# Performance work log

Measured on AMD Instinct MI355X. Metric: run time of the kernel, lower is better.

## Reference

```python
import jax, jax.numpy as jnp
import numpy as np

ITER_NUM = 3
BN_EPS = 1e-5
L2_EPS = 1e-12


def setup_inputs() -> dict:
    key = jax.random.key(0)
    k1, k2 = jax.random.split(key, 2)
    B, C, h, w = 64, 256, 14, 14
    E = 512
    feat = jax.random.normal(k1, (B, C, h, w), dtype=jnp.float32)
    W_proj = jax.random.normal(k2, (E, C * C), dtype=jnp.float32) * (1.0 / np.sqrt(C * C))
    b_proj = jnp.zeros((E,), dtype=jnp.float32)
    bn_gamma = jnp.ones((E,), dtype=jnp.float32)
    bn_beta = jnp.zeros((E,), dtype=jnp.float32)
    bn_mean = jnp.zeros((E,), dtype=jnp.float32)
    bn_var = jnp.ones((E,), dtype=jnp.float32)
    return {"feat": feat, "W_proj": W_proj, "b_proj": b_proj,
            "bn_gamma": bn_gamma, "bn_beta": bn_beta,
            "bn_mean": bn_mean, "bn_var": bn_var}


def _mpncov(feat):
    # feat: [B, C, h, w] -> [B, C, C] matrix square root of normalized covariance
    B, C, h, w = feat.shape
    M = h * w
    x = feat.reshape(B, C, M)
    # I_hat = I - (1/M) * ones  (centering matrix)
    I_hat = jnp.eye(M, dtype=feat.dtype) - (1.0 / M) * jnp.ones((M, M), dtype=feat.dtype)
    # y = x @ I_hat @ x^T / M  -> [B, C, C]
    xc = jnp.einsum('bcm,mn->bcn', x, I_hat)
    y = jnp.einsum('bcm,bdm->bcd', xc, x) / M
    trY = jnp.trace(y, axis1=-2, axis2=-1)  # [B]
    y = y / trY[:, None, None]
    I = jnp.broadcast_to(jnp.eye(C, dtype=feat.dtype), (B, C, C))
    Y, Z = y, I
    for _ in range(ITER_NUM):
        ZY = jnp.einsum('bij,bjk->bik', Z, Y)
        T = 3.0 * I - ZY
        Y = 0.5 * jnp.einsum('bij,bjk->bik', Y, T)
        Z = 0.5 * jnp.einsum('bij,bjk->bik', T, Z)
    return Y * jnp.sqrt(trY)[:, None, None]


def _l2_normalize(x, axis=-1):
    n = jnp.sqrt(jnp.sum(x * x, axis=axis, keepdims=True))
    return x / jnp.maximum(n, L2_EPS)


def reference(feat, W_proj, b_proj, bn_gamma, bn_beta, bn_mean, bn_var):
    B = feat.shape[0]
    pooled = _mpncov(feat)                      # [B, C, C]
    flat = pooled.reshape(B, -1)                # [B, C*C]
    flat = _l2_normalize(flat, axis=1)
    # dropout in eval mode = identity
    emb = flat @ W_proj.T + b_proj              # [B, E]
    # BatchNorm1d (inference mode, running stats)
    emb = (emb - bn_mean) * jax.lax.rsqrt(bn_var + BN_EPS) * bn_gamma + bn_beta
    norm_embedding = _l2_normalize(emb, axis=1)
    return norm_embedding
```

## Files before the change

### kernel.cpp

```cpp
#include <hip/hip_runtime.h>
#include <hip/hip_bf16.h>

#define BATCH 64
#define CDIM  256
#define MHW   196
#define MP    224
#define EDIM  512
#define CC    65536
#define NTRI  10

typedef __attribute__((ext_vector_type(8))) short short8_t;
typedef __attribute__((ext_vector_type(4))) float f32x4;
typedef __attribute__((ext_vector_type(4))) unsigned int u32x4;

static __device__ __forceinline__ short f2bf(float f) {
    __hip_bfloat16 h = __float2bfloat16(f);
    return (short)__builtin_bit_cast(unsigned short, h);
}

struct MMOp {
    const __hip_bfloat16* A;
    const __hip_bfloat16* B;
    const __hip_bfloat16* D;
    __hip_bfloat16*       out;
    const float*          alpha_ptr;
    int                   alpha_mode;
    float                 alpha_c, beta, gamma;
    float*                nrm;
};

__global__ __launch_bounds__(256) void k_center(const float* __restrict__ feat,
                                                __hip_bfloat16* __restrict__ xcb,
                                                float* __restrict__ rowsq)
{
    const int row = blockIdx.x * 4 + (threadIdx.x >> 6);
    const int l = threadIdx.x & 63;
    const float* src = feat + (size_t)row * MHW;
    float v0 = src[l];
    float v1 = src[l + 64];
    float v2 = src[l + 128];
    float v3 = (l + 192 < MHW) ? src[l + 192] : 0.0f;
    float s = v0 + v1 + v2 + v3;
    #pragma unroll
    for (int o = 32; o >= 1; o >>= 1) s += __shfl_xor(s, o, 64);
    const float mean = s * (1.0f / MHW);
    v0 -= mean; v1 -= mean; v2 -= mean;
    v3 = (l + 192 < MHW) ? (v3 - mean) : 0.0f;
    float sq = v0*v0 + v1*v1 + v2*v2 + v3*v3;
    #pragma unroll
    for (int o = 32; o >= 1; o >>= 1) sq += __shfl_xor(sq, o, 64);
    if (l == 0) rowsq[row] = sq;
    __hip_bfloat16* dst = xcb + (size_t)row * MP;
    dst[l]       = __float2bfloat16(v0);
    dst[l + 64]  = __float2bfloat16(v1);
    dst[l + 128] = __float2bfloat16(v2);
    if (l + 192 < MP) dst[l + 192] = __float2bfloat16(v3);
}

template<int KT, bool NORM>
__global__ __launch_bounds__(256) void k_mm(MMOp op0, MMOp op1)
{
    const MMOp& op = (blockIdx.y == 0) ? op0 : op1;

    __shared__ __hip_bfloat16 As[64][72];
    __shared__ __hip_bfloat16 Bs[64][72];
    __shared__ float red[4];
    __shared__ float s_alpha;

    const int b = blockIdx.x / NTRI;
    const int t = blockIdx.x - b * NTRI;
    int ti, tj;
    if (t < 4)      { ti = 0; tj = t; }
    else if (t < 7) { ti = 1; tj = t - 3; }
    else if (t < 9) { ti = 2; tj = t - 5; }
    else            { ti = 3; tj = 3; }

    const int tid = threadIdx.x;
    const int wv = tid >> 6, l = tid & 63;
    const int wr = wv >> 1, wc = wv & 1;
    const int lr = l & 15,  lg = l >> 4;

    if (op.alpha_mode) {
        float v = op.alpha_ptr[b * 256 + tid];
        #pragma unroll
        for (int o = 32; o >= 1; o >>= 1) v += __shfl_xor(v, o, 64);
        if (l == 0) red[wv] = v;
        __syncthreads();
        if (tid == 0) s_alpha = op.alpha_c / (red[0] + red[1] + red[2] + red[3]);
    } else if (tid == 0) {
        s_alpha = op.alpha_c;
    }

    const __hip_bfloat16* Ab = op.A + (size_t)b * (CDIM * KT) + (size_t)ti * 64 * KT;
    const __hip_bfloat16* Bb = op.B + (size_t)b * (CDIM * KT) + (size_t)tj * 64 * KT;

    f32x4 acc[2][2];
    #pragma unroll
    for (int i = 0; i < 2; i++)
        #pragma unroll
        for (int j = 0; j < 2; j++)
            #pragma unroll
            for (int r = 0; r < 4; r++) acc[i][j][r] = 0.0f;

    #pragma unroll
    for (int k0 = 0; k0 < KT; k0 += 64) {
        const int kw   = (KT - k0 >= 64) ? 64 : (KT - k0);
        const int segs = kw >> 3;
        __syncthreads();
        for (int u = tid; u < 64 * segs; u += 256) {
            const int row = u / segs;
            const int seg = u - row * segs;
            *reinterpret_cast<u32x4*>(&As[row][seg * 8]) =
                *reinterpret_cast<const u32x4*>(Ab + (size_t)row * KT + k0 + seg * 8);
            *reinterpret_cast<u32x4*>(&Bs[row][seg * 8]) =
                *reinterpret_cast<const u32x4*>(Bb + (size_t)row * KT + k0 + seg * 8);
        }
        __syncthreads();
        const int nks = kw >> 5;
        for (int ks = 0; ks < nks; ks++) {
            short8_t af[2], bfr[2];
            #pragma unroll
            for (int i = 0; i < 2; i++)
                af[i] = *reinterpret_cast<const short8_t*>(&As[wr * 32 + i * 16 + lr][ks * 32 + lg * 8]);
            #pragma unroll
            for (int j = 0; j < 2; j++)
                bfr[j] = *reinterpret_cast<const short8_t*>(&Bs[wc * 32 + j * 16 + lr][ks * 32 + lg * 8]);
            #pragma unroll
            for (int i = 0; i < 2; i++)
                #pragma unroll
                for (int j = 0; j < 2; j++)
                    acc[i][j] = __builtin_amdgcn_mfma_f32_16x16x32_bf16(af[i], bfr[j], acc[i][j], 0, 0, 0);
        }
    }

    const float a = s_alpha;
    __hip_bfloat16* ob = op.out + (size_t)b * CC;
    const __hip_bfloat16* Db = op.D ? (op.D + (size_t)b * CC) : nullptr;
    float ns = 0.0f;
    #pragma unroll
    for (int i = 0; i < 2; i++) {
        #pragma unroll
        for (int j = 0; j < 2; j++) {
            #pragma unroll
            for (int r = 0; r < 4; r++) {
                const int grow = ti * 64 + wr * 32 + i * 16 + lg * 4 + r;
                const int gcol = tj * 64 + wc * 32 + j * 16 + lr;
                float v = a * acc[i][j][r];
                if (Db) v += op.beta * __bfloat162float(Db[grow * 256 + gcol]);
                if (grow == gcol) v += op.gamma;
                const __hip_bfloat16 hv = __float2bfloat16(v);
                ob[grow * 256 + gcol] = hv;
                if (ti != tj) ob[gcol * 256 + grow] = hv;
                if (NORM) {
                    const float fv = __bfloat162float(hv);
                    ns += ((ti != tj) ? 2.0f : 1.0f) * fv * fv;
                }
            }
        }
    }
    if constexpr (NORM) {
        #pragma unroll
        for (int o = 32; o >= 1; o >>= 1) ns += __shfl_xor(ns, o, 64);
        __syncthreads();
        if (l == 0) red[wv] = ns;
        __syncthreads();
        if (tid == 0) op.nrm[b * NTRI + t] = red[0] + red[1] + red[2] + red[3];
    }
}

__global__ __launch_bounds__(256) void k_proj(const __hip_bfloat16* __restrict__ flat,
                                              const float* __restrict__ W,
                                              float* __restrict__ upart)
{
    const int ks = blockIdx.x;
    const int et = blockIdx.y;
    const int tid = threadIdx.x, wv = tid >> 6, l = tid & 63;
    const int lr = l & 15, lg = l >> 4;
    const int kbase = ks * 2048 + wv * 512;

    f32x4 acc[4][4];
    #pragma unroll
    for (int i = 0; i < 4; i++)
        #pragma unroll
        for (int j = 0; j < 4; j++)
            #pragma unroll
            for (int r = 0; r < 4; r++) acc[i][j][r] = 0.0f;

    for (int kk = 0; kk < 512; kk += 32) {
        const int k = kbase + kk + lg * 8;
        short8_t af[4];
        #pragma unroll
        for (int i = 0; i < 4; i++)
            af[i] = *reinterpret_cast<const short8_t*>(flat + (size_t)(i * 16 + lr) * CC + k);
        short8_t bfr[4];
        #pragma unroll
        for (int j = 0; j < 4; j++) {
            const f32x4* wp = reinterpret_cast<const f32x4*>(W + (size_t)(et * 64 + j * 16 + lr) * CC + k);
            const f32x4 w0 = wp[0], w1 = wp[1];
            short8_t s;
            s[0] = f2bf(w0[0]); s[1] = f2bf(w0[1]); s[2] = f2bf(w0[2]); s[3] = f2bf(w0[3]);
            s[4] = f2bf(w1[0]); s[5] = f2bf(w1[1]); s[6] = f2bf(w1[2]); s[7] = f2bf(w1[3]);
            bfr[j] = s;
        }
        #pragma unroll
        for (int i = 0; i < 4; i++)
            #pragma unroll
            for (int j = 0; j < 4; j++)
                acc[i][j] = __builtin_amdgcn_mfma_f32_16x16x32_bf16(af[i], bfr[j], acc[i][j], 0, 0, 0);
    }

    __shared__ float racc[2][64][65];
    if (wv >= 2) {
        #pragma unroll
        for (int i = 0; i < 4; i++)
            #pragma unroll
            for (int j = 0; j < 4; j++)
                #pragma unroll
                for (int r = 0; r < 4; r++)
                    racc[wv - 2][i * 16 + lg * 4 + r][j * 16 + lr] = acc[i][j][r];
    }
    __syncthreads();
    if (wv < 2) {
        #pragma unroll
        for (int i = 0; i < 4; i++)
            #pragma unroll
            for (int j = 0; j < 4; j++)
                #pragma unroll
                for (int r = 0; r < 4; r++)
                    racc[wv][i * 16 + lg * 4 + r][j * 16 + lr] += acc[i][j][r];
    }
    __syncthreads();
    float* ub = upart + (size_t)ks * (64 * EDIM);
    #pragma unroll
    for (int q = 0; q < 16; q++) {
        const int idx = q * 256 + tid;
        const int x = idx >> 6, y = idx & 63;
        ub[(size_t)x * EDIM + et * 64 + y] = racc[0][x][y] + racc[1][x][y];
    }
}

__global__ __launch_bounds__(512) void k_final(const float* __restrict__ upart,
                                               const float* __restrict__ nrmp,
                                               const float* __restrict__ bias,
                                               const float* __restrict__ gma,
                                               const float* __restrict__ bta,
                                               const float* __restrict__ mu,
                                               const float* __restrict__ var,
                                               float* __restrict__ out)
{
    const int b = blockIdx.x;
    const int e = threadIdx.x;
    float u = 0.0f;
    for (int p = 0; p < 32; p++)
        u += upart[((size_t)p * 64 + b) * EDIM + e];
    float fro = 0.0f;
    #pragma unroll
    for (int q = 0; q < NTRI; q++) fro += nrmp[b * NTRI + q];
    const float s = 1.0f / fmaxf(sqrtf(fro), 1e-12f);
    const float emb = s * u + bias[e];
    const float v = (emb - mu[e]) * rsqrtf(var[e] + 1e-5f) * gma[e] + bta[e];
    float sq = v * v;
    #pragma unroll
    for (int o = 32; o >= 1; o >>= 1) sq += __shfl_xor(sq, o, 64);
    __shared__ float wsum[8];
    if ((e & 63) == 0) wsum[e >> 6] = sq;
    __syncthreads();
    float tot = 0.0f;
    #pragma unroll
    for (int i = 0; i < 8; i++) tot += wsum[i];
    out[(size_t)b * EDIM + e] = v / fmaxf(sqrtf(tot), 1e-12f);
}

extern "C" void kernel_launch(void* const* d_in, const int* in_sizes, int n_in,
                              void* d_out, int out_size, void* d_ws, size_t ws_size,
                              hipStream_t stream)
{
    const float* feat = (const float*)d_in[0];
    const float* W    = (const float*)d_in[1];
    const float* bias = (const float*)d_in[2];
    const float* gma  = (const float*)d_in[3];
    const float* bta  = (const float*)d_in[4];
    const float* mu   = (const float*)d_in[5];
    const float* var  = (const float*)d_in[6];
    float* out = (float*)d_out;

    char* ws = (char*)d_ws;
    constexpr size_t XCB_BYTES = (size_t)BATCH * CDIM * MP * 2;
    constexpr size_t MATB      = (size_t)BATCH * CC * 2;
    constexpr size_t OFF_ROWSQ = 4096;
    constexpr size_t OFF_XCB   = OFF_ROWSQ + (size_t)BATCH * CDIM * 4;
    constexpr size_t OFF_M     = OFF_XCB + XCB_BYTES;
    constexpr size_t OFF_UP    = OFF_M + 5 * MATB;
    constexpr size_t NEEDED    = OFF_UP + (size_t)32 * 64 * EDIM * 4;
    if (ws_size < NEEDED) return;

    float* nrmp  = (float*)(ws + 1024);
    float* rowsq = (float*)(ws + OFF_ROWSQ);
    __hip_bfloat16* xcb = (__hip_bfloat16*)(ws + OFF_XCB);
    __hip_bfloat16* M0  = (__hip_bfloat16*)(ws + OFF_M + 0 * MATB);
    __hip_bfloat16* M1  = (__hip_bfloat16*)(ws + OFF_M + 1 * MATB);
    __hip_bfloat16* M2  = (__hip_bfloat16*)(ws + OFF_M + 2 * MATB);
    __hip_bfloat16* M3  = (__hip_bfloat16*)(ws + OFF_M + 3 * MATB);
    __hip_bfloat16* M4  = (__hip_bfloat16*)(ws + OFF_M + 4 * MATB);
    float* upart = (float*)(ws + OFF_UP);

    k_center<<<dim3(4096), dim3(256), 0, stream>>>(feat, xcb, rowsq);

    const dim3 g1(BATCH * NTRI, 1), g2(BATCH * NTRI, 2), blk(256);
    MMOp nop = {};

    MMOp cov = {xcb, xcb, nullptr, M0, rowsq, 1, 1.0f, 0.0f, 0.0f, nullptr};
    k_mm<MP, false><<<g1, blk, 0, stream>>>(cov, nop);
    MMOp y1 = {M0, M0, M0, M1, nullptr, 0, -0.5f, 1.5f, 0.0f, nullptr};
    k_mm<256, false><<<g1, blk, 0, stream>>>(y1, nop);
    MMOp t2 = {M0, M1, M1, M2, nullptr, 0, 0.5f, -1.5f, 3.0f, nullptr};
    k_mm<256, false><<<g1, blk, 0, stream>>>(t2, nop);
    MMOp y2 = {M1, M2, nullptr, M3, nullptr, 0, 0.5f, 0.0f, 0.0f, nullptr};
    MMOp z2 = {M2, M0, M2, M4, nullptr, 0, -0.25f, 0.75f, 0.0f, nullptr};
    k_mm<256, false><<<g2, blk, 0, stream>>>(y2, z2);
    MMOp t3 = {M4, M3, nullptr, M1, nullptr, 0, -1.0f, 0.0f, 3.0f, nullptr};
    k_mm<256, false><<<g1, blk, 0, stream>>>(t3, nop);
    MMOp y3 = {M3, M1, nullptr, M2, nullptr, 0, 0.5f, 0.0f, 0.0f, nrmp};
    k_mm<256, true ><<<g1, blk, 0, stream>>>(y3, nop);

    k_proj<<<dim3(32, 8), blk, 0, stream>>>(M2, W, upart);
    k_final<<<dim3(64), 512, 0, stream>>>(upart, nrmp, bias, gma, bta, mu, var, out);
}
```

Measured before the change: 133.1 us.

## Fuse centering and Newton-Schulz chain into one per-batch megakernel with W pre-conversion

New measurement: 287.5 us. +116.0%, slower.

```diff
diff --git a/kernel.cpp b/kernel.cpp
--- a/kernel.cpp
+++ b/kernel.cpp
@@ -8,34 +8,21 @@
 #define EDIM  512
 #define CC    65536
 #define NTRI  10
+#define WCONV_BLOCKS 2048
 
 typedef __attribute__((ext_vector_type(8))) short short8_t;
 typedef __attribute__((ext_vector_type(4))) float f32x4;
-typedef __attribute__((ext_vector_type(4))) unsigned int u32x4;
-
-static __device__ __forceinline__ short f2bf(float f) {
+
+static __device__ __forceinline__ unsigned short f2bfu(float f) {
     __hip_bfloat16 h = __float2bfloat16(f);
-    return (short)__builtin_bit_cast(unsigned short, h);
-}
-
-struct MMOp {
-    const __hip_bfloat16* A;
-    const __hip_bfloat16* B;
-    const __hip_bfloat16* D;
-    __hip_bfloat16*       out;
-    const float*          alpha_ptr;
-    int                   alpha_mode;
-    float                 alpha_c, beta, gamma;
-    float*                nrm;
-};
-
-__global__ __launch_bounds__(256) void k_center(const float* __restrict__ feat,
-                                                __hip_bfloat16* __restrict__ xcb,
-                                                float* __restrict__ rowsq)
-{
-    const int row = blockIdx.x * 4 + (threadIdx.x >> 6);
-    const int l = threadIdx.x & 63;
-    const float* src = feat + (size_t)row * MHW;
+    return __builtin_bit_cast(unsigned short, h);
+}
+
+static __device__ __forceinline__ void center_row(
+    const float* __restrict__ feat_b, __hip_bfloat16* __restrict__ xcb_b,
+    float* __restrict__ rs, int row, int l)
+{
+    const float* src = feat_b + (size_t)row * MHW;
     float v0 = src[l];
     float v1 = src[l + 64];
     float v2 = src[l + 128];
@@ -49,8 +36,8 @@
     float sq = v0*v0 + v1*v1 + v2*v2 + v3*v3;
     #pragma unroll
     for (int o = 32; o >= 1; o >>= 1) sq += __shfl_xor(sq, o, 64);
-    if (l == 0) rowsq[row] = sq;
-    __hip_bfloat16* dst = xcb + (size_t)row * MP;
+    if (l == 0) rs[row] = sq;
+    __hip_bfloat16* dst = xcb_b + (size_t)row * MP;
     dst[l]       = __float2bfloat16(v0);
     dst[l + 64]  = __float2bfloat16(v1);
     dst[l + 128] = __float2bfloat16(v2);
@@ -58,99 +45,59 @@
 }
 
 template<int KT, bool NORM>
-__global__ __launch_bounds__(256) void k_mm(MMOp op0, MMOp op1)
-{
-    const MMOp& op = (blockIdx.y == 0) ? op0 : op1;
-
-    __shared__ __hip_bfloat16 As[64][72];
-    __shared__ __hip_bfloat16 Bs[64][72];
-    __shared__ float red[4];
-    __shared__ float s_alpha;
-
-    const int b = blockIdx.x / NTRI;
-    const int t = blockIdx.x - b * NTRI;
+static __device__ __forceinline__ float mm64(
+    const __hip_bfloat16* __restrict__ A, const __hip_bfloat16* __restrict__ Bm,
+    const __hip_bfloat16* __restrict__ D, __hip_bfloat16* __restrict__ out,
+    float a, float beta, float gamma, int t, int l)
+{
     int ti, tj;
     if (t < 4)      { ti = 0; tj = t; }
     else if (t < 7) { ti = 1; tj = t - 3; }
     else if (t < 9) { ti = 2; tj = t - 5; }
     else            { ti = 3; tj = 3; }
-
-    const int tid = threadIdx.x;
-    const int wv = tid >> 6, l = tid & 63;
-    const int wr = wv >> 1, wc = wv & 1;
-    const int lr = l & 15,  lg = l >> 4;
-
-    if (op.alpha_mode) {
-        float v = op.alpha_ptr[b * 256 + tid];
-        #pragma unroll
-        for (int o = 32; o >= 1; o >>= 1) v += __shfl_xor(v, o, 64);
-        if (l == 0) red[wv] = v;
-        __syncthreads();
-        if (tid == 0) s_alpha = op.alpha_c / (red[0] + red[1] + red[2] + red[3]);
-    } else if (tid == 0) {
-        s_alpha = op.alpha_c;
-    }
-
-    const __hip_bfloat16* Ab = op.A + (size_t)b * (CDIM * KT) + (size_t)ti * 64 * KT;
-    const __hip_bfloat16* Bb = op.B + (size_t)b * (CDIM * KT) + (size_t)tj * 64 * KT;
-
-    f32x4 acc[2][2];
-    #pragma unroll
-    for (int i = 0; i < 2; i++)
-        #pragma unroll
-        for (int j = 0; j < 2; j++)
+    const int lr = l & 15, lg = l >> 4;
+
+    f32x4 acc[4][4];
+    #pragma unroll
+    for (int i = 0; i < 4; i++)
+        #pragma unroll
+        for (int j = 0; j < 4; j++)
             #pragma unroll
             for (int r = 0; r < 4; r++) acc[i][j][r] = 0.0f;
 
-    #pragma unroll
-    for (int k0 = 0; k0 < KT; k0 += 64) {
-        const int kw   = (KT - k0 >= 64) ? 64 : (KT - k0);
-        const int segs = kw >> 3;
-        __syncthreads();
-        for (int u = tid; u < 64 * segs; u += 256) {
-            const int row = u / segs;
-            const int seg = u - row * segs;
-            *reinterpret_cast<u32x4*>(&As[row][seg * 8]) =
-                *reinterpret_cast<const u32x4*>(Ab + (size_t)row * KT + k0 + seg * 8);
-            *reinterpret_cast<u32x4*>(&Bs[row][seg * 8]) =
-                *reinterpret_cast<const u32x4*>(Bb + (size_t)row * KT + k0 + seg * 8);
-        }
-        __syncthreads();
-        const int nks = kw >> 5;
-        for (int ks = 0; ks < nks; ks++) {
-            short8_t af[2], bfr[2];
-            #pragma unroll
-            for (int i = 0; i < 2; i++)
-                af[i] = *reinterpret_cast<const short8_t*>(&As[wr * 32 + i * 16 + lr][ks * 32 + lg * 8]);
-            #pragma unroll
-            for (int j = 0; j < 2; j++)
-                bfr[j] = *reinterpret_cast<const short8_t*>(&Bs[wc * 32 + j * 16 + lr][ks * 32 + lg * 8]);
-            #pragma unroll
-            for (int i = 0; i < 2; i++)
-                #pragma unroll
-                for (int j = 0; j < 2; j++)
-                    acc[i][j] = __builtin_amdgcn_mfma_f32_16x16x32_bf16(af[i], bfr[j], acc[i][j], 0, 0, 0);
-        }
-    }
-
-    const float a = s_alpha;
-    __hip_bfloat16* ob = op.out + (size_t)b * CC;
-    const __hip_bfloat16* Db = op.D ? (op.D + (size_t)b * CC) : nullptr;
+    const __hip_bfloat16* Ab = A  + (size_t)(ti * 64 + lr) * KT;
+    const __hip_bfloat16* Bb = Bm + (size_t)(tj * 64 + lr) * KT;
+    for (int k0 = 0; k0 < KT; k0 += 32) {
+        const int k = k0 + lg * 8;
+        short8_t af[4], bfr[4];
+        #pragma unroll
+        for (int i = 0; i < 4; i++)
+            af[i] = *reinterpret_cast<const short8_t*>(Ab + (size_t)i * 16 * KT + k);
+        #pragma unroll
+        for (int j = 0; j < 4; j++)
+            bfr[j] = *reinterpret_cast<const short8_t*>(Bb + (size_t)j * 16 * KT + k);
+        #pragma unroll
+        for (int i = 0; i < 4; i++)
+            #pragma unroll
+            for (int j = 0; j < 4; j++)
+                acc[i][j] = __builtin_amdgcn_mfma_f32_16x16x32_bf16(af[i], bfr[j], acc[i][j], 0, 0, 0);
+    }
+
     float ns = 0.0f;
     #pragma unroll
-    for (int i = 0; i < 2; i++) {
-        #pragma unroll
-        for (int j = 0; j < 2; j++) {
+    for (int i = 0; i < 4; i++) {
+        #pragma unroll
+        for (int j = 0; j < 4; j++) {
             #pragma unroll
             for (int r = 0; r < 4; r++) {
-                const int grow = ti * 64 + wr * 32 + i * 16 + lg * 4 + r;
-                const int gcol = tj * 64 + wc * 32 + j * 16 + lr;
+                const int grow = ti * 64 + i * 16 + lg * 4 + r;
+                const int gcol = tj * 64 + j * 16 + lr;
                 float v = a * acc[i][j][r];
-                if (Db) v += op.beta * __bfloat162float(Db[grow * 256 + gcol]);
-                if (grow == gcol) v += op.gamma;
+                if (D) v += beta * __bfloat162float(D[grow * 256 + gcol]);
+                if (grow == gcol) v += gamma;
                 const __hip_bfloat16 hv = __float2bfloat16(v);
-                ob[grow * 256 + gcol] = hv;
-                if (ti != tj) ob[gcol * 256 + grow] = hv;
+                out[grow * 256 + gcol] = hv;
+                if (ti != tj) out[gcol * 256 + grow] = hv;
                 if (NORM) {
                     const float fv = __bfloat162float(hv);
                     ns += ((ti != tj) ? 2.0f : 1.0f) * fv * fv;
@@ -158,25 +105,95 @@
             }
         }
     }
-    if constexpr (NORM) {
-        #pragma unroll
-        for (int o = 32; o >= 1; o >>= 1) ns += __shfl_xor(ns, o, 64);
-        __syncthreads();
-        if (l == 0) red[wv] = ns;
-        __syncthreads();
-        if (tid == 0) op.nrm[b * NTRI + t] = red[0] + red[1] + red[2] + red[3];
-    }
-}
-
-__global__ __launch_bounds__(256) void k_proj(const __hip_bfloat16* __restrict__ flat,
-                                              const float* __restrict__ W,
-                                              float* __restrict__ upart)
-{
-    const int ks = blockIdx.x;
-    const int et = blockIdx.y;
+    return ns;
+}
+
+__global__ __launch_bounds__(1024) void k_mega(
+    const float* __restrict__ feat, const float* __restrict__ W,
+    __hip_bfloat16* __restrict__ xcb_all, __hip_bfloat16* __restrict__ Wbf,
+    __hip_bfloat16* __restrict__ M0, __hip_bfloat16* __restrict__ M1,
+    __hip_bfloat16* __restrict__ M2, __hip_bfloat16* __restrict__ M3,
+    __hip_bfloat16* __restrict__ M4, float* __restrict__ nrm)
+{
+    const int tid = threadIdx.x, w = tid >> 6, l = tid & 63;
+
+    if (blockIdx.x >= BATCH) {
+        const size_t base = (size_t)(blockIdx.x - BATCH) * 16384;
+        #pragma unroll
+        for (int it = 0; it < 4; ++it) {
+            const size_t idx = base + (size_t)it * 4096 + (size_t)tid * 4;
+            const f32x4 v = *reinterpret_cast<const f32x4*>(W + idx);
+            ushort4 o;
+            o.x = f2bfu(v[0]); o.y = f2bfu(v[1]); o.z = f2bfu(v[2]); o.w = f2bfu(v[3]);
+            *reinterpret_cast<ushort4*>(Wbf + idx) = o;
+        }
+        return;
+    }
+
+    __shared__ float rs[256];
+    __shared__ float red[16];
+    __shared__ float s_alpha;
+
+    const int b = blockIdx.x;
+    const float* feat_b = feat + (size_t)b * CDIM * MHW;
+    __hip_bfloat16* xcb = xcb_all + (size_t)b * CDIM * MP;
+    __hip_bfloat16* m0 = M0 + (size_t)b * CC;
+    __hip_bfloat16* m1 = M1 + (size_t)b * CC;
+    __hip_bfloat16* m2 = M2 + (size_t)b * CC;
+    __hip_bfloat16* m3 = M3 + (size_t)b * CC;
+    __hip_bfloat16* m4 = M4 + (size_t)b * CC;
+
+    #pragma unroll
+    for (int it = 0; it < 16; ++it)
+        center_row(feat_b, xcb, rs, it * 16 + w, l);
+    __syncthreads();
+
+    if (tid < 256) {
+        float v = rs[tid];
+        #pragma unroll
+        for (int o = 32; o >= 1; o >>= 1) v += __shfl_xor(v, o, 64);
+        if (l == 0) red[tid >> 6] = v;
+    }
+    __syncthreads();
+    if (tid == 0) s_alpha = 1.0f / (red[0] + red[1] + red[2] + red[3]);
+    __syncthreads();
+
+    if (w < NTRI) mm64<MP,  false>(xcb, xcb, nullptr, m0, s_alpha, 0.0f, 0.0f, w, l);
+    __syncthreads();
+    if (w < NTRI) mm64<256, false>(m0, m0, m0, m1, -0.5f, 1.5f, 0.0f, w, l);
+    __syncthreads();
+    if (w < NTRI) mm64<256, false>(m0, m1, m1, m2, 0.5f, -1.5f, 3.0f, w, l);
+    __syncthreads();
+    if (w < NTRI) {
+        mm64<256, false>(m1, m2, nullptr, m3, 0.5f, 0.0f, 0.0f, w, l);
+        mm64<256, false>(m2, m0, m2, m4, -0.25f, 0.75f, 0.0f, w, l);
+    }
+    __syncthreads();
+    if (w < NTRI) mm64<256, false>(m4, m3, nullptr, m1, -1.0f, 0.0f, 3.0f, w, l);
+    __syncthreads();
+    float ns = 0.0f;
+    if (w < NTRI) ns = mm64<256, true>(m3, m1, nullptr, m2, 0.5f, 0.0f, 0.0f, w, l);
+    #pragma unroll
+    for (int o = 32; o >= 1; o >>= 1) ns += __shfl_xor(ns, o, 64);
+    if (l == 0) red[w] = ns;
+    __syncthreads();
+    if (tid == 0) {
+        float f = 0.0f;
+        #pragma unroll
+        for (int q = 0; q < NTRI; ++q) f += red[q];
+        nrm[b] = f;
+    }
+}
+
+__global__ __launch_bounds__(256) void k_proj2(const __hip_bfloat16* __restrict__ flat,
+                                               const __hip_bfloat16* __restrict__ Wbf,
+                                               float* __restrict__ upart)
+{
+    __shared__ float racc[2][64][65];
+    const int ks = blockIdx.x, et = blockIdx.y;
     const int tid = threadIdx.x, wv = tid >> 6, l = tid & 63;
     const int lr = l & 15, lg = l >> 4;
-    const int kbase = ks * 2048 + wv * 512;
+    const int kbase = ks * 1024 + wv * 256;
 
     f32x4 acc[4][4];
     #pragma unroll
@@ -186,22 +203,15 @@
             #pragma unroll
             for (int r = 0; r < 4; r++) acc[i][j][r] = 0.0f;
 
-    for (int kk = 0; kk < 512; kk += 32) {
+    for (int kk = 0; kk < 256; kk += 32) {
         const int k = kbase + kk + lg * 8;
-        short8_t af[4];
+        short8_t af[4], bfr[4];
         #pragma unroll
         for (int i = 0; i < 4; i++)
             af[i] = *reinterpret_cast<const short8_t*>(flat + (size_t)(i * 16 + lr) * CC + k);
-        short8_t bfr[4];
-        #pragma unroll
-        for (int j = 0; j < 4; j++) {
-            const f32x4* wp = reinterpret_cast<const f32x4*>(W + (size_t)(et * 64 + j * 16 + lr) * CC + k);
-            const f32x4 w0 = wp[0], w1 = wp[1];
-            short8_t s;
-            s[0] = f2bf(w0[0]); s[1] = f2bf(w0[1]); s[2] = f2bf(w0[2]); s[3] = f2bf(w0[3]);
-            s[4] = f2bf(w1[0]); s[5] = f2bf(w1[1]); s[6] = f2bf(w1[2]); s[7] = f2bf(w1[3]);
-            bfr[j] = s;
-        }
+        #pragma unroll
+        for (int j = 0; j < 4; j++)
+            bfr[j] = *reinterpret_cast<const short8_t*>(Wbf + (size_t)(et * 64 + j * 16 + lr) * CC + k);
         #pragma unroll
         for (int i = 0; i < 4; i++)
             #pragma unroll
@@ -209,7 +219,6 @@
                 acc[i][j] = __builtin_amdgcn_mfma_f32_16x16x32_bf16(af[i], bfr[j], acc[i][j], 0, 0, 0);
     }
 
-    __shared__ float racc[2][64][65];
     if (wv >= 2) {
         #pragma unroll
         for (int i = 0; i < 4; i++)
@@ -239,36 +248,38 @@
     }
 }
 
-__global__ __launch_bounds__(512) void k_final(const float* __restrict__ upart,
-                                               const float* __restrict__ nrmp,
-                                               const float* __restrict__ bias,
-                                               const float* __restrict__ gma,
-                                               const float* __restrict__ bta,
-                                               const float* __restrict__ mu,
-                                               const float* __restrict__ var,
-                                               float* __restrict__ out)
-{
-    const int b = blockIdx.x;
-    const int e = threadIdx.x;
-    float u = 0.0f;
-    for (int p = 0; p < 32; p++)
-        u += upart[((size_t)p * 64 + b) * EDIM + e];
-    float fro = 0.0f;
-    #pragma unroll
-    for (int q = 0; q < NTRI; q++) fro += nrmp[b * NTRI + q];
-    const float s = 1.0f / fmaxf(sqrtf(fro), 1e-12f);
-    const float emb = s * u + bias[e];
-    const float v = (emb - mu[e]) * rsqrtf(var[e] + 1e-5f) * gma[e] + bta[e];
-    float sq = v * v;
+__global__ __launch_bounds__(256) void k_fin(const float* __restrict__ upart,
+                                             const float* __restrict__ nrm,
+                                             const float* __restrict__ bias,
+                                             const float* __restrict__ gma,
+                                             const float* __restrict__ bta,
+                                             const float* __restrict__ mu,
+                                             const float* __restrict__ var,
+                                             float* __restrict__ out)
+{
+    __shared__ float wsum[4];
+    const int bb = blockIdx.x;
+    const int tid = threadIdx.x, wv = tid >> 6, l = tid & 63;
+    const int e0 = tid, e1 = tid + 256;
+    float u0 = 0.0f, u1 = 0.0f;
+    for (int p = 0; p < 64; ++p) {
+        const float* up = upart + ((size_t)p * 64 + bb) * EDIM;
+        u0 += up[e0]; u1 += up[e1];
+    }
+    const float s = 1.0f / fmaxf(sqrtf(nrm[bb]), 1e-12f);
+    const float emb0 = s * u0 + bias[e0];
+    const float emb1 = s * u1 + bias[e1];
+    const float v0 = (emb0 - mu[e0]) * rsqrtf(var[e0] + 1e-5f) * gma[e0] + bta[e0];
+    const float v1 = (emb1 - mu[e1]) * rsqrtf(var[e1] + 1e-5f) * gma[e1] + bta[e1];
+    float sq = v0 * v0 + v1 * v1;
     #pragma unroll
     for (int o = 32; o >= 1; o >>= 1) sq += __shfl_xor(sq, o, 64);
-    __shared__ float wsum[8];
-    if ((e & 63) == 0) wsum[e >> 6] = sq;
-    __syncthreads();
-    float tot = 0.0f;
-    #pragma unroll
-    for (int i = 0; i < 8; i++) tot += wsum[i];
-    out[(size_t)b * EDIM + e] = v / fmaxf(sqrtf(tot), 1e-12f);
+    if (l == 0) wsum[wv] = sq;
+    __syncthreads();
+    const float tot = wsum[0] + wsum[1] + wsum[2] + wsum[3];
+    const float rn = 1.0f / fmaxf(sqrtf(tot), 1e-12f);
+    out[(size_t)bb * EDIM + e0] = v0 * rn;
+    out[(size_t)bb * EDIM + e1] = v1 * rn;
 }
 
 extern "C" void kernel_launch(void* const* d_in, const int* in_sizes, int n_in,
@@ -287,42 +298,26 @@
     char* ws = (char*)d_ws;
     constexpr size_t XCB_BYTES = (size_t)BATCH * CDIM * MP * 2;
     constexpr size_t MATB      = (size_t)BATCH * CC * 2;
-    constexpr size_t OFF_ROWSQ = 4096;
-    constexpr size_t OFF_XCB   = OFF_ROWSQ + (size_t)BATCH * CDIM * 4;
+    constexpr size_t WBF_BYTES = (size_t)CC * EDIM * 2;
+    constexpr size_t OFF_XCB   = 4096;
     constexpr size_t OFF_M     = OFF_XCB + XCB_BYTES;
-    constexpr size_t OFF_UP    = OFF_M + 5 * MATB;
-    constexpr size_t NEEDED    = OFF_UP + (size_t)32 * 64 * EDIM * 4;
+    constexpr size_t OFF_WBF   = OFF_M + 5 * MATB;
+    constexpr size_t OFF_UP    = OFF_WBF + WBF_BYTES;
+    constexpr size_t NEEDED    = OFF_UP + (size_t)64 * 64 * EDIM * 4;
     if (ws_size < NEEDED) return;
 
-    float* nrmp  = (float*)(ws + 1024);
-    float* rowsq = (float*)(ws + OFF_ROWSQ);
+    float* nrm = (float*)(ws + 0);
     __hip_bfloat16* xcb = (__hip_bfloat16*)(ws + OFF_XCB);
     __hip_bfloat16* M0  = (__hip_bfloat16*)(ws + OFF_M + 0 * MATB);
     __hip_bfloat16* M1  = (__hip_bfloat16*)(ws + OFF_M + 1 * MATB);
     __hip_bfloat16* M2  = (__hip_bfloat16*)(ws + OFF_M + 2 * MATB);
     __hip_bfloat16* M3  = (__hip_bfloat16*)(ws + OFF_M + 3 * MATB);
     __hip_bfloat16* M4  = (__hip_bfloat16*)(ws + OFF_M + 4 * MATB);
+    __hip_bfloat16* Wbf = (__hip_bfloat16*)(ws + OFF_WBF);
     float* upart = (float*)(ws + OFF_UP);
 
-    k_center<<<dim3(4096), dim3(256), 0, stream>>>(feat, xcb, rowsq);
-
-    const dim3 g1(BATCH * NTRI, 1), g2(BATCH * NTRI, 2), blk(256);
-    MMOp nop = {};
-
-    MMOp cov = {xcb, xcb, nullptr, M0, rowsq, 1, 1.0f, 0.0f, 0.0f, nullptr};
-    k_mm<MP, false><<<g1, blk, 0, stream>>>(cov, nop);
-    MMOp y1 = {M0, M0, M0, M1, nullptr, 0, -0.5f, 1.5f, 0.0f, nullptr};
-    k_mm<256, false><<<g1, blk, 0, stream>>>(y1, nop);
-    MMOp t2 = {M0, M1, M1, M2, nullptr, 0, 0.5f, -1.5f, 3.0f, nullptr};
-    k_mm<256, false><<<g1, blk, 0, stream>>>(t2, nop);
-    MMOp y2 = {M1, M2, nullptr, M3, nullptr, 0, 0.5f, 0.0f, 0.0f, nullptr};
-    MMOp z2 = {M2, M0, M2, M4, nullptr, 0, -0.25f, 0.75f, 0.0f, nullptr};
-    k_mm<256, false><<<g2, blk, 0, stream>>>(y2, z2);
-    MMOp t3 = {M4, M3, nullptr, M1, nullptr, 0, -1.0f, 0.0f, 3.0f, nullptr};
-    k_mm<256, false><<<g1, blk, 0, stream>>>(t3, nop);
-    MMOp y3 = {M3, M1, nullptr, M2, nullptr, 0, 0.5f, 0.0f, 0.0f, nrmp};
-    k_mm<256, true ><<<g1, blk, 0, stream>>>(y3, nop);
-
-    k_proj<<<dim3(32, 8), blk, 0, stream>>>(M2, W, upart);
-    k_final<<<dim3(64), 512, 0, stream>>>(upart, nrmp, bias, gma, bta, mu, var, out);
-}
+    k_mega<<<dim3(BATCH + WCONV_BLOCKS), dim3(1024), 0, stream>>>(
+        feat, W, xcb, Wbf, M0, M1, M2, M3, M4, nrm);
+    k_proj2<<<dim3(64, 8), dim3(256), 0, stream>>>(M2, Wbf, upart);
+    k_fin<<<dim3(64), dim3(256), 0, stream>>>(upart, nrm, bias, gma, bta, mu, var, out);
+}
```
